# Performance work log

Measured on AMD Instinct MI355X. Metric: run time of the kernel, lower is better.

## Reference

```python
import jax, jax.numpy as jnp
import numpy as np


def setup_inputs() -> dict:
    key = jax.random.key(0)
    ks = jax.random.split(key, 4)
    B, T, D, U = 64, 2048, 128, 128
    enc = jax.random.normal(ks[0], (B, T, D), dtype=jnp.float32)
    # Keras Dense default: glorot_uniform kernel, zero bias; use scaled normals here.
    W1_w = jax.random.normal(ks[1], (D, U), dtype=jnp.float32) / np.sqrt(D)
    W2_w = jax.random.normal(ks[2], (D, U), dtype=jnp.float32) / np.sqrt(D)
    V_w = jax.random.normal(ks[3], (U, 1), dtype=jnp.float32) / np.sqrt(U)
    return {
        "encoder_outputs": enc,
        "W1_w": W1_w,
        "W1_b": jnp.zeros((U,), jnp.float32),
        "W2_w": W2_w,
        "W2_b": jnp.zeros((U,), jnp.float32),
        "V_w": V_w,
        "V_b": jnp.zeros((1,), jnp.float32),
    }


def reference(encoder_outputs, W1_w, W1_b, W2_w, W2_b, V_w, V_b):
    # score = V(tanh(W1(x) + W2(x)))  -> [B, T, 1]
    # W1(x)+W2(x) == x @ (W1_w + W2_w) + (W1_b + W2_b); keep faithful but fused.
    h = jnp.tanh(jnp.einsum("btd,du->btu", encoder_outputs, W1_w) + W1_b
                 + jnp.einsum("btd,du->btu", encoder_outputs, W2_w) + W2_b)
    score = jnp.einsum("btu,uo->bto", h, V_w) + V_b  # [B, T, 1]
    attn = jax.nn.softmax(score, axis=1)             # softmax over sequence axis
    # context = sum_t attn[b,t,0] * x[b,t,:]
    context = jnp.einsum("bto,btd->bd", attn, encoder_outputs)
    return context
```

## Files before the change

kernel.cpp:

```cpp
#include <hip/hip_runtime.h>
#include <hip/hip_bf16.h>

#define DD 128
#define UU 128
#define SEQ_T 2048
#define ROWS 128
#define PART_STRIDE 132

typedef __attribute__((ext_vector_type(8))) short short8;
typedef __attribute__((ext_vector_type(4))) float f32x4;

__device__ __forceinline__ unsigned short f2bf(float f) {
  unsigned u = __float_as_uint(f);
  u += 0x7fffu + ((u >> 16) & 1u);
  return (unsigned short)(u >> 16);
}
__device__ __forceinline__ float bf2f(unsigned short s) {
  return __uint_as_float(((unsigned)s) << 16);
}
__device__ __forceinline__ float fast_tanh(float v) {
  float z = __expf(2.0f * v);
  return 1.0f - __fdividef(2.0f, z + 1.0f);
}

__global__ void prep_kernel(const float* __restrict__ W1w, const float* __restrict__ W1b,
                            const float* __restrict__ W2w, const float* __restrict__ W2b,
                            unsigned short* __restrict__ wt_g, float* __restrict__ bias_g)
{
  int i = blockIdx.x * 256 + threadIdx.x;
  int u = i >> 7, d = i & 127;
  float s = W1w[(size_t)d * UU + u] + W2w[(size_t)d * UU + u];
  wt_g[(size_t)u * DD + d] = f2bf(s);
  if (i < UU) bias_g[i] = W1b[i] + W2b[i];
}

__global__ __launch_bounds__(256, 2)
void fused_score_ctx(const float* __restrict__ x,
                     const unsigned short* __restrict__ wt_g,
                     const float* __restrict__ bias_g,
                     const float* __restrict__ Vw,
                     float* __restrict__ part)
{
  __shared__ __align__(16) unsigned short xs[ROWS * DD];
  __shared__ __align__(16) unsigned short wt[UU * DD];
  __shared__ float bsum[UU];
  __shared__ float vv[UU];
  __shared__ float slds[ROWS];
  __shared__ float pctx[2 * DD];
  __shared__ float red[8];

  const int tid = threadIdx.x;
  const int blk = blockIdx.x;
  const int rowbase = blk * ROWS;

  if (tid < UU) { bsum[tid] = bias_g[tid]; vv[tid] = Vw[tid]; }

  #pragma unroll
  for (int it = 0; it < 8; ++it) {
    int F = tid + 256 * it;
    int row = F >> 4, g = F & 15;
    const float* src = x + (size_t)(rowbase + row) * DD + g * 8;
    const float4 v0 = *reinterpret_cast<const float4*>(src);
    const float4 v1 = *reinterpret_cast<const float4*>(src + 4);
    short8 pk;
    pk[0] = (short)f2bf(v0.x); pk[1] = (short)f2bf(v0.y);
    pk[2] = (short)f2bf(v0.z); pk[3] = (short)f2bf(v0.w);
    pk[4] = (short)f2bf(v1.x); pk[5] = (short)f2bf(v1.y);
    pk[6] = (short)f2bf(v1.z); pk[7] = (short)f2bf(v1.w);
    *reinterpret_cast<short8*>(xs + row * DD + ((g ^ (row & 15)) << 3)) = pk;
  }
  #pragma unroll
  for (int it = 0; it < 8; ++it) {
    int F = tid + 256 * it;
    int u = F >> 4, g = F & 15;
    short8 wv = *reinterpret_cast<const short8*>(wt_g + (size_t)F * 8);
    *reinterpret_cast<short8*>(wt + u * DD + ((g ^ (u & 15)) << 3)) = wv;
  }
  __syncthreads();

  const int w = tid >> 6, l = tid & 63, lx = l & 15, lq = l >> 4;
  f32x4 acc[2][8];
  #pragma unroll
  for (int mf = 0; mf < 2; ++mf)
    #pragma unroll
    for (int nf = 0; nf < 8; ++nf) acc[mf][nf] = (f32x4){0.f, 0.f, 0.f, 0.f};

  const int arow0 = w * 32 + lx;
  #pragma unroll
  for (int kf = 0; kf < 4; ++kf) {
    const int gs8 = ((kf * 4 + lq) ^ lx) << 3;
    short8 a0 = *reinterpret_cast<const short8*>(xs + arow0 * DD + gs8);
    short8 a1 = *reinterpret_cast<const short8*>(xs + (arow0 + 16) * DD + gs8);
    short8 b[8];
    #pragma unroll
    for (int nf = 0; nf < 8; ++nf)
      b[nf] = *reinterpret_cast<const short8*>(wt + (nf * 16 + lx) * DD + gs8);
    #pragma unroll
    for (int nf = 0; nf < 8; ++nf) {
      acc[0][nf] = __builtin_amdgcn_mfma_f32_16x16x32_bf16(a0, b[nf], acc[0][nf], 0, 0, 0);
      acc[1][nf] = __builtin_amdgcn_mfma_f32_16x16x32_bf16(a1, b[nf], acc[1][nf], 0, 0, 0);
    }
  }

  float vs[8], bs[8];
  #pragma unroll
  for (int nf = 0; nf < 8; ++nf) { vs[nf] = vv[nf * 16 + lx]; bs[nf] = bsum[nf * 16 + lx]; }
  #pragma unroll
  for (int mf = 0; mf < 2; ++mf) {
    #pragma unroll
    for (int r = 0; r < 4; ++r) {
      float p = 0.0f;
      #pragma unroll
      for (int nf = 0; nf < 8; ++nf)
        p += vs[nf] * fast_tanh(acc[mf][nf][r] + bs[nf]);
      p += __shfl_xor(p, 1);
      p += __shfl_xor(p, 2);
      p += __shfl_xor(p, 4);
      p += __shfl_xor(p, 8);
      if (lx == 0) slds[w * 32 + mf * 16 + lq * 4 + r] = p;
    }
  }
  __syncthreads();

  float sv = slds[tid & 127];
  float m = sv;
  #pragma unroll
  for (int off = 1; off < 64; off <<= 1) m = fmaxf(m, __shfl_xor(m, off));
  if ((tid & 63) == 0) red[tid >> 6] = m;
  __syncthreads();
  m = fmaxf(fmaxf(red[0], red[1]), fmaxf(red[2], red[3]));

  float e = (tid < 128) ? __expf(sv - m) : 0.0f;
  float lsum = e;
  #pragma unroll
  for (int off = 1; off < 64; off <<= 1) lsum += __shfl_xor(lsum, off);
  if ((tid & 63) == 0) red[4 + (tid >> 6)] = lsum;
  __syncthreads();
  lsum = (red[4] + red[5]) + (red[6] + red[7]);

  if (tid < 128) slds[tid] = e;
  __syncthreads();

  const int d = tid & 127, half = tid >> 7;
  const int gd = d >> 3, el = d & 7;
  float ca = 0.0f;
  #pragma unroll 8
  for (int k = 0; k < 64; ++k) {
    int t = half * 64 + k;
    float wgt = slds[t];
    ca = fmaf(wgt, bf2f(xs[t * DD + (((gd ^ (t & 15)) << 3) + el)]), ca);
  }
  pctx[half * 128 + d] = ca;
  __syncthreads();

  float* prec = part + (size_t)blk * PART_STRIDE;
  if (tid < 128) prec[4 + tid] = pctx[tid] + pctx[128 + tid];
  if (tid == 0) { prec[0] = m; prec[1] = lsum; }
}

__global__ void combine_kernel(const float* __restrict__ part,
                               float* __restrict__ out, int chunks)
{
  int b = blockIdx.x;
  int d = threadIdx.x;
  float mg = -3.0e38f;
  for (int i = 0; i < chunks; ++i)
    mg = fmaxf(mg, part[(size_t)(b * chunks + i) * PART_STRIDE]);
  float den = 0.0f, num = 0.0f;
  for (int i = 0; i < chunks; ++i) {
    const float* p = part + (size_t)(b * chunks + i) * PART_STRIDE;
    float sc = __expf(p[0] - mg);
    den = fmaf(sc, p[1], den);
    num = fmaf(sc, p[4 + d], num);
  }
  out[(size_t)b * DD + d] = __fdividef(num, den);
}

extern "C" void kernel_launch(void* const* d_in, const int* in_sizes, int n_in,
                              void* d_out, int out_size, void* d_ws, size_t ws_size,
                              hipStream_t stream)
{
  const float* x   = (const float*)d_in[0];
  const float* W1w = (const float*)d_in[1];
  const float* W1b = (const float*)d_in[2];
  const float* W2w = (const float*)d_in[3];
  const float* W2b = (const float*)d_in[4];
  const float* Vw  = (const float*)d_in[5];

  const int bt = in_sizes[0] / DD;
  const int nblk = bt / ROWS;
  const int B = bt / SEQ_T;
  const int chunks = SEQ_T / ROWS;

  float* part = (float*)d_ws;
  unsigned short* wt_g = (unsigned short*)((char*)d_ws + 540672);
  float* bias_g = (float*)((char*)d_ws + 540672 + 32768);

  prep_kernel<<<64, 256, 0, stream>>>(W1w, W1b, W2w, W2b, wt_g, bias_g);
  fused_score_ctx<<<nblk, 256, 0, stream>>>(x, wt_g, bias_g, Vw, part);
  combine_kernel<<<B, 128, 0, stream>>>(part, (float*)d_out, chunks);
}
```

Baseline: 44.68 us.

## Read weight tile from global, drop LDS copy, vectorize context reduction

The LDS copy of the fused weight matrix is removed, and MFMA B operands are now loaded directly from global/L2. This halves shared memory per block, and launch bounds are raised to 4 blocks per CU for higher occupancy. The context accumulation is rewritten so each thread reads 8 bf16 values as a vector and the partial sums are reduced with shuffles across 16-thread groups. The trade-off is repeated global loads of the weights per block, which rely on cache hits, and possible register pressure under the tighter launch bound.

```diff
diff --git a/kernel.cpp b/kernel.cpp
--- a/kernel.cpp
+++ b/kernel.cpp
@@ -34,7 +34,7 @@
   if (i < UU) bias_g[i] = W1b[i] + W2b[i];
 }
 
-__global__ __launch_bounds__(256, 2)
+__global__ __launch_bounds__(256, 4)
 void fused_score_ctx(const float* __restrict__ x,
                      const unsigned short* __restrict__ wt_g,
                      const float* __restrict__ bias_g,
@@ -42,11 +42,10 @@
                      float* __restrict__ part)
 {
   __shared__ __align__(16) unsigned short xs[ROWS * DD];
-  __shared__ __align__(16) unsigned short wt[UU * DD];
   __shared__ float bsum[UU];
   __shared__ float vv[UU];
   __shared__ float slds[ROWS];
-  __shared__ float pctx[2 * DD];
+  __shared__ float pctx_red[4][DD];
   __shared__ float red[8];
 
   const int tid = threadIdx.x;
@@ -69,13 +68,6 @@
     pk[6] = (short)f2bf(v1.z); pk[7] = (short)f2bf(v1.w);
     *reinterpret_cast<short8*>(xs + row * DD + ((g ^ (row & 15)) << 3)) = pk;
   }
-  #pragma unroll
-  for (int it = 0; it < 8; ++it) {
-    int F = tid + 256 * it;
-    int u = F >> 4, g = F & 15;
-    short8 wv = *reinterpret_cast<const short8*>(wt_g + (size_t)F * 8);
-    *reinterpret_cast<short8*>(wt + u * DD + ((g ^ (u & 15)) << 3)) = wv;
-  }
   __syncthreads();
 
   const int w = tid >> 6, l = tid & 63, lx = l & 15, lq = l >> 4;
@@ -94,7 +86,8 @@
     short8 b[8];
     #pragma unroll
     for (int nf = 0; nf < 8; ++nf)
-      b[nf] = *reinterpret_cast<const short8*>(wt + (nf * 16 + lx) * DD + gs8);
+      b[nf] = *reinterpret_cast<const short8*>(
+          wt_g + (size_t)(nf * 16 + lx) * DD + (kf * 4 + lq) * 8);
     #pragma unroll
     for (int nf = 0; nf < 8; ++nf) {
       acc[0][nf] = __builtin_amdgcn_mfma_f32_16x16x32_bf16(a0, b[nf], acc[0][nf], 0, 0, 0);
@@ -141,20 +134,39 @@
   if (tid < 128) slds[tid] = e;
   __syncthreads();
 
-  const int d = tid & 127, half = tid >> 7;
-  const int gd = d >> 3, el = d & 7;
-  float ca = 0.0f;
-  #pragma unroll 8
-  for (int k = 0; k < 64; ++k) {
-    int t = half * 64 + k;
-    float wgt = slds[t];
-    ca = fmaf(wgt, bf2f(xs[t * DD + (((gd ^ (t & 15)) << 3) + el)]), ca);
-  }
-  pctx[half * 128 + d] = ca;
+  {
+    const int gd = tid & 15;
+    const int tg = tid >> 4;
+    float ca[8];
+    #pragma unroll
+    for (int e2 = 0; e2 < 8; ++e2) ca[e2] = 0.0f;
+    #pragma unroll
+    for (int k = 0; k < 8; ++k) {
+      int t = tg * 8 + k;
+      float wgt = slds[t];
+      short8 xv = *reinterpret_cast<const short8*>(xs + t * DD + ((gd ^ (t & 15)) << 3));
+      #pragma unroll
+      for (int e2 = 0; e2 < 8; ++e2)
+        ca[e2] = fmaf(wgt, bf2f((unsigned short)xv[e2]), ca[e2]);
+    }
+    #pragma unroll
+    for (int e2 = 0; e2 < 8; ++e2) {
+      ca[e2] += __shfl_xor(ca[e2], 16);
+      ca[e2] += __shfl_xor(ca[e2], 32);
+    }
+    if ((l >> 4) == 0) {
+      #pragma unroll
+      for (int e2 = 0; e2 < 8; ++e2) pctx_red[w][gd * 8 + e2] = ca[e2];
+    }
+  }
   __syncthreads();
 
   float* prec = part + (size_t)blk * PART_STRIDE;
-  if (tid < 128) prec[4 + tid] = pctx[tid] + pctx[128 + tid];
+  if (tid < 128) {
+    float c0 = (pctx_red[0][tid] + pctx_red[1][tid]) +
+               (pctx_red[2][tid] + pctx_red[3][tid]);
+    prec[4 + tid] = c0;
+  }
   if (tid == 0) { prec[0] = m; prec[1] = lsum; }
 }
 
```

Measured after the change: 53.73 us. +20.2%, slower.
